# Kernel optimization log

Hardware: AMD Instinct MI355X
Metric: run time of the kernel (lower is better)

## Reference

```python
import jax, jax.numpy as jnp
import numpy as np
import math

FACTOR = 5

def setup_inputs() -> dict:
    key = jax.random.key(0)
    k1, k2, k3, k4 = jax.random.split(key, 4)
    B, L, H, D = 2, 4096, 8, 64
    sample_k = min(FACTOR * int(np.ceil(np.log(L))), L)  # 45
    return {
        "queries": jax.random.normal(k1, (B, L, H, D), dtype=jnp.float32),
        "keys": jax.random.normal(k2, (B, L, H, D), dtype=jnp.float32),
        "values": jax.random.normal(k3, (B, L, H, D), dtype=jnp.float32),
        "attn_mask": jnp.zeros((1,), dtype=bool),  # unused (mask_flag=False)
        "index_sample": jax.random.randint(k4, (L, sample_k), 0, L, dtype=jnp.int64),
    }

def reference(queries, keys, values, attn_mask, index_sample):
    B, L_Q, H, D = queries.shape
    L_K = keys.shape[1]
    # [B,L,H,D] -> [B,H,L,D]
    q = jnp.transpose(queries, (0, 2, 1, 3))
    k = jnp.transpose(keys, (0, 2, 1, 3))
    v = jnp.transpose(values, (0, 2, 1, 3))

    n_top = min(FACTOR * int(np.ceil(np.log(L_Q))), L_Q)  # u

    # --- _prob_QK ---
    # K_sample[b,h,l,s,e] = k[b,h,index_sample[l,s],e]
    K_sample = k[:, :, index_sample, :]                      # [B,H,L_Q,S,E]
    Q_K_sample = jnp.einsum('bhle,bhlse->bhls', q, K_sample)  # [B,H,L_Q,S]
    # sparsity measure: max - mean(over full L_K as in torch code)
    M = Q_K_sample.max(axis=-1) - Q_K_sample.sum(axis=-1) / L_K  # [B,H,L_Q]
    M_top = jax.lax.top_k(M, n_top)[1]                        # [B,H,u] indices

    Q_reduce = jnp.take_along_axis(q, M_top[..., None], axis=2)  # [B,H,u,E]
    scores_top = jnp.einsum('bhue,bhke->bhuk', Q_reduce, k)      # [B,H,u,L_K]

    scale = 1.0 / math.sqrt(D)
    attn = jax.nn.softmax(scale * scores_top, axis=-1)           # [B,H,u,L_K]
    context_in_q = jnp.einsum('bhuk,bhkd->bhud', attn, v)        # [B,H,u,D]

    # scatter selected contexts into zero-initialized tensor
    b_idx = jnp.arange(B)[:, None, None]
    h_idx = jnp.arange(H)[None, :, None]
    context = jnp.zeros((B, H, L_Q, D), dtype=queries.dtype)
    context = context.at[b_idx, h_idx, M_top].set(context_in_q)

    return jnp.transpose(context, (0, 2, 1, 3))  # [B,L_Q,H,D]
```

## Files before the change

kernel.cpp:

```cpp
#include <hip/hip_runtime.h>
#include <math.h>

#define B_ 2
#define L_ 4096
#define H_ 8
#define D_ 64
#define S_ 45
#define NTOP_ 45
#define SCALE 0.125f
#define TKEYS 64
#define NSPLIT 64

__global__ __launch_bounds__(256) void compute_M_kernel(
    const float* __restrict__ q, const float* __restrict__ k,
    const int* __restrict__ samp, float* __restrict__ M) {
    __shared__ int sIdx[4 * 48];
    int tid = threadIdx.x;
    int g   = blockIdx.x;
    int xcd = g & 7;
    int s0  = g >> 3;
    int b   = xcd >> 2;
    int chunk = (xcd & 3) + 4 * s0;
    int l0  = chunk * 4;

    if (tid < 4 * S_) {
        int qq = tid / S_, ss = tid - qq * S_;
        sIdx[qq * 48 + ss] = samp[(long)(l0 + qq) * S_ + ss];
    }
    if (tid < 12) sIdx[(tid / 3) * 48 + S_ + (tid % 3)] = 0;
    __syncthreads();

    int lane = tid & 63, w = tid >> 6;
    int l = l0 + w;
    int h = lane >> 3, part = lane & 7;

    const float4* qrow = (const float4*)(q + ((long)(b * L_ + l)) * (H_ * D_));
    float4 qa = qrow[2 * lane], qb = qrow[2 * lane + 1];

    const float4* kb4 = (const float4*)(k + (long)b * L_ * (H_ * D_));
    const int* myIdx = sIdx + w * 48;

    const float4* r0 = kb4 + (long)myIdx[0] * (H_ * D_ / 4);
    float4 ka0 = r0[2 * lane], kb0 = r0[2 * lane + 1];
    const float4* r1 = kb4 + (long)myIdx[1] * (H_ * D_ / 4);
    float4 ka1 = r1[2 * lane], kb1 = r1[2 * lane + 1];

    float vmax = -INFINITY, vsum = 0.f;
    #pragma unroll 3
    for (int s = 0; s < S_; ++s) {
        int nidx = myIdx[s + 2];
        const float4* nr = kb4 + (long)nidx * (H_ * D_ / 4);
        float4 na = nr[2 * lane], nb = nr[2 * lane + 1];

        float p = qa.x * ka0.x + qa.y * ka0.y + qa.z * ka0.z + qa.w * ka0.w
                + qb.x * kb0.x + qb.y * kb0.y + qb.z * kb0.z + qb.w * kb0.w;
        p += __shfl_xor(p, 1, 64);
        p += __shfl_xor(p, 2, 64);
        p += __shfl_xor(p, 4, 64);
        vmax = fmaxf(vmax, p);
        vsum += p;

        ka0 = ka1; kb0 = kb1;
        ka1 = na;  kb1 = nb;
    }
    if (part == 0)
        M[((long)(b * H_ + h)) * L_ + l] = vmax - vsum * (1.0f / (float)L_);
}

__global__ __launch_bounds__(256) void topk_kernel(
    const float* __restrict__ M, int* __restrict__ topIdx) {
    __shared__ unsigned int hist[256];
    __shared__ unsigned int suf[257];
    __shared__ unsigned int wsum[4];
    __shared__ int sBin, sRemain, sCnt, sTieCnt;
    __shared__ int tie[64];

    int bh = blockIdx.x, tid = threadIdx.x;
    int lane = tid & 63, wave = tid >> 6;
    const float* row = M + (long)bh * L_;

    unsigned int key[16];
    #pragma unroll
    for (int j = 0; j < 16; ++j) {
        unsigned int bts = __float_as_uint(row[tid + 256 * j]);
        key[j] = bts ^ ((unsigned int)((int)bts >> 31) | 0x80000000u);
    }

    unsigned int prefix = 0, pmask = 0;
    int remain = NTOP_;
    #pragma unroll 1
    for (int pass = 3; pass >= 0; --pass) {
        int shift = pass * 8;
        hist[tid] = 0;
        __syncthreads();
        #pragma unroll
        for (int j = 0; j < 16; ++j) {
            if ((key[j] & pmask) == prefix)
                atomicAdd(&hist[(key[j] >> shift) & 255u], 1u);
        }
        __syncthreads();
        unsigned int s = hist[tid];
        #pragma unroll
        for (int off = 1; off < 64; off <<= 1) {
            unsigned int o = __shfl_down(s, off, 64);
            if (lane + off < 64) s += o;
        }
        if (lane == 0) wsum[wave] = s;
        __syncthreads();
        unsigned int add = 0;
        for (int w = wave + 1; w < 4; ++w) add += wsum[w];
        s += add;
        suf[tid] = s;
        if (tid == 0) suf[256] = 0;
        __syncthreads();
        if (suf[tid] >= (unsigned int)remain && suf[tid + 1] < (unsigned int)remain) {
            sBin = tid;
            sRemain = remain - (int)suf[tid + 1];
        }
        __syncthreads();
        prefix |= ((unsigned int)sBin) << shift;
        pmask  |= 0xFFu << shift;
        remain  = sRemain;
        __syncthreads();
    }

    if (tid == 0) { sCnt = 0; sTieCnt = 0; }
    __syncthreads();
    int* outRow = topIdx + bh * NTOP_;
    #pragma unroll
    for (int j = 0; j < 16; ++j) {
        int idx = tid + 256 * j;
        if (key[j] > prefix) {
            int pos = atomicAdd(&sCnt, 1);
            outRow[pos] = idx;
        } else if (key[j] == prefix) {
            int tp = atomicAdd(&sTieCnt, 1);
            if (tp < 64) tie[tp] = idx;
        }
    }
    __syncthreads();
    if (tid == 0) {
        int base = sCnt;
        int tc = sTieCnt < 64 ? sTieCnt : 64;
        for (int t = 0; t < remain; ++t) {
            int mi = 0x7fffffff, mj = 0;
            for (int j2 = 0; j2 < tc; ++j2)
                if (tie[j2] < mi) { mi = tie[j2]; mj = j2; }
            outRow[base + t] = mi;
            tie[mj] = 0x7fffffff;
        }
    }
}

#define STRIDE 68
__global__ __launch_bounds__(256, 2) void attn_strip_kernel(
    const float* __restrict__ q, const float* __restrict__ k,
    const float* __restrict__ v, const int* __restrict__ topIdx,
    float* __restrict__ pOut, float* __restrict__ plPart, int nsplit) {
    __shared__ float sQ[48 * STRIDE];
    __shared__ float sK[TKEYS * STRIDE];
    __shared__ float sV[TKEYS * STRIDE];
    __shared__ float sP[48 * STRIDE];

    int g = blockIdx.x;
    int xcd = g & 7;
    int s0 = g >> 3;
    int grp = s0 / nsplit;
    int bh = xcd + 8 * grp;
    int split = s0 - grp * nsplit;
    int b = bh >> 3, h = bh & 7;
    int tid = threadIdx.x;
    int key0 = split * TKEYS;

    #pragma unroll
    for (int j = 0; j < 3; ++j) {
        int i = tid + 256 * j;
        int u = i >> 4, d4 = i & 15;
        float4 val = make_float4(0.f, 0.f, 0.f, 0.f);
        if (u < NTOP_) {
            int lq = topIdx[bh * NTOP_ + u];
            val = *(const float4*)(q + (((long)(b * L_ + lq)) * H_ + h) * D_ + 4 * d4);
        }
        *(float4*)(sQ + u * STRIDE + 4 * d4) = val;
    }
    #pragma unroll
    for (int j = 0; j < 4; ++j) {
        int i = tid + 256 * j;
        int r = i >> 4, d4 = i & 15;
        long off = (((long)(b * L_ + key0 + r)) * H_ + h) * D_ + 4 * d4;
        *(float4*)(sK + r * STRIDE + 4 * d4) = *(const float4*)(k + off);
        *(float4*)(sV + r * STRIDE + 4 * d4) = *(const float4*)(v + off);
    }
    __syncthreads();

    int tx = tid & 15, ty = tid >> 4;
    float acc[3][4];
    #pragma unroll
    for (int i = 0; i < 3; ++i)
        #pragma unroll
        for (int j = 0; j < 4; ++j) acc[i][j] = 0.f;

    #pragma unroll 4
    for (int d4 = 0; d4 < 16; ++d4) {
        float4 qv[3];
        #pragma unroll
        for (int i = 0; i < 3; ++i)
            qv[i] = *(const float4*)(sQ + (3 * ty + i) * STRIDE + 4 * d4);
        #pragma unroll
        for (int j = 0; j < 4; ++j) {
            float4 kv = *(const float4*)(sK + (tx + 16 * j) * STRIDE + 4 * d4);
            #pragma unroll
            for (int i = 0; i < 3; ++i)
                acc[i][j] += qv[i].x * kv.x + qv[i].y * kv.y + qv[i].z * kv.z + qv[i].w * kv.w;
        }
    }
    #pragma unroll
    for (int i = 0; i < 3; ++i) {
        #pragma unroll
        for (int j = 0; j < 4; ++j)
            sP[(3 * ty + i) * STRIDE + tx + 16 * j] = __expf(acc[i][j] * SCALE);
    }
    __syncthreads();

    int dx = tid & 15, uy = tid >> 4;
    float o[3][4];
    float ls[3];
    #pragma unroll
    for (int i = 0; i < 3; ++i) {
        ls[i] = 0.f;
        #pragma unroll
        for (int c = 0; c < 4; ++c) o[i][c] = 0.f;
    }
    #pragma unroll 4
    for (int k4 = 0; k4 < 16; ++k4) {
        float pa[3][4];
        #pragma unroll
        for (int i = 0; i < 3; ++i)
            *(float4*)pa[i] = *(const float4*)(sP + (3 * uy + i) * STRIDE + 4 * k4);
        #pragma unroll
        for (int c = 0; c < 4; ++c) {
            float4 vr = *(const float4*)(sV + (4 * k4 + c) * STRIDE + 4 * dx);
            #pragma unroll
            for (int i = 0; i < 3; ++i) {
                o[i][0] += pa[i][c] * vr.x;
                o[i][1] += pa[i][c] * vr.y;
                o[i][2] += pa[i][c] * vr.z;
                o[i][3] += pa[i][c] * vr.w;
                ls[i]   += pa[i][c];
            }
        }
    }
    #pragma unroll
    for (int i = 0; i < 3; ++i) {
        int u = 3 * uy + i;
        if (u < NTOP_) {
            long base = ((long)(split * 16 + bh) * NTOP_ + u) * D_;
            *(float4*)(pOut + base + 4 * dx) = make_float4(o[i][0], o[i][1], o[i][2], o[i][3]);
            if (dx == 0) plPart[(long)(split * 16 + bh) * NTOP_ + u] = ls[i];
        }
    }
}

__global__ __launch_bounds__(256) void reduce_norm_kernel(
    const int* __restrict__ topIdx, const float* __restrict__ pOut,
    const float* __restrict__ plPart, float* __restrict__ out, int nsplit) {
    __shared__ float part[4][64];
    __shared__ float lpart[4];
    int u = blockIdx.x, bh = blockIdx.y;
    int b = bh >> 3, h = bh & 7;
    int tid = threadIdx.x;
    int d = tid & 63, sg = tid >> 6;
    float acc = 0.f, lsum = 0.f;
    for (int s = sg; s < nsplit; s += 4) {
        acc  += pOut[((long)(s * 16 + bh) * NTOP_ + u) * D_ + d];
        lsum += plPart[(long)(s * 16 + bh) * NTOP_ + u];
    }
    part[sg][d] = acc;
    if (d == 0) lpart[sg] = lsum;
    __syncthreads();
    if (sg == 0) {
        float a = part[0][d] + part[1][d] + part[2][d] + part[3][d];
        float lt = lpart[0] + lpart[1] + lpart[2] + lpart[3];
        int lq = topIdx[bh * NTOP_ + u];
        out[(((long)(b * L_ + lq)) * H_ + h) * D_ + d] = a / lt;
    }
}

extern "C" void kernel_launch(void* const* d_in, const int* in_sizes, int n_in,
                              void* d_out, int out_size, void* d_ws, size_t ws_size,
                              hipStream_t stream) {
    const float* q = (const float*)d_in[0];
    const float* k = (const float*)d_in[1];
    const float* v = (const float*)d_in[2];
    const int* samp = (const int*)d_in[4];
    float* out = (float*)d_out;

    char* ws = (char*)d_ws;
    const size_t mBytes   = (size_t)B_ * H_ * L_ * sizeof(float);
    const size_t topBytes = (size_t)B_ * H_ * NTOP_ * sizeof(int);
    const size_t plBytes  = (size_t)NSPLIT * 16 * NTOP_ * sizeof(float);
    float* M      = (float*)ws;
    int*   topIdx = (int*)(ws + mBytes);
    float* plPart = (float*)(ws + mBytes + topBytes);
    float* pOut   = (float*)(ws + mBytes + topBytes + plBytes);

    int nsplit = NSPLIT;
    while (nsplit > 1) {
        size_t need = mBytes + topBytes + plBytes +
                      (size_t)nsplit * 16 * NTOP_ * D_ * sizeof(float);
        if (need <= ws_size) break;
        nsplit >>= 1;
    }

    hipMemsetAsync(d_out, 0, (size_t)out_size * sizeof(float), stream);

    compute_M_kernel<<<2048, 256, 0, stream>>>(q, k, samp, M);

    topk_kernel<<<B_ * H_, 256, 0, stream>>>(M, topIdx);

    attn_strip_kernel<<<nsplit * B_ * H_, 256, 0, stream>>>(
        q, k, v, topIdx, pOut, plPart, nsplit);

    dim3 gn(NTOP_, B_ * H_);
    reduce_norm_kernel<<<gn, 256, 0, stream>>>(topIdx, pOut, plPart, out, nsplit);
}
```

Baseline: 184.8 us.

## Split compute_M work across head-pairs so each wave handles two queries

Restructures the sampled QK sparsity kernel so each block covers 8 queries for one pair of heads (128 floats) rather than 4 queries across all heads. Each half-wave loads a single float4 per sampled key row instead of two and reduces over 16 lanes, and the grid doubles to 4096 blocks. The intent is more parallelism and a smaller per-thread register and load footprint, with the XCD mapping keyed to head-pair. In exchange the sample index table is loaded twice as often and each block reads narrower 512-byte segments of every key row.

```diff
diff --git a/kernel.cpp b/kernel.cpp
--- a/kernel.cpp
+++ b/kernel.cpp
@@ -14,57 +14,57 @@
 __global__ __launch_bounds__(256) void compute_M_kernel(
     const float* __restrict__ q, const float* __restrict__ k,
     const int* __restrict__ samp, float* __restrict__ M) {
-    __shared__ int sIdx[4 * 48];
+    __shared__ int sIdx[8 * 48];
     int tid = threadIdx.x;
     int g   = blockIdx.x;
     int xcd = g & 7;
-    int s0  = g >> 3;
+    int blk = g >> 3;
     int b   = xcd >> 2;
-    int chunk = (xcd & 3) + 4 * s0;
-    int l0  = chunk * 4;
-
-    if (tid < 4 * S_) {
-        int qq = tid / S_, ss = tid - qq * S_;
+    int hp  = xcd & 3;
+    int l0  = blk * 8;
+
+    for (int i = tid; i < 8 * S_; i += 256) {
+        int qq = i / S_, ss = i - qq * S_;
         sIdx[qq * 48 + ss] = samp[(long)(l0 + qq) * S_ + ss];
     }
-    if (tid < 12) sIdx[(tid / 3) * 48 + S_ + (tid % 3)] = 0;
+    if (tid < 24) sIdx[(tid / 3) * 48 + S_ + (tid % 3)] = 0;
     __syncthreads();
 
     int lane = tid & 63, w = tid >> 6;
-    int l = l0 + w;
-    int h = lane >> 3, part = lane & 7;
-
-    const float4* qrow = (const float4*)(q + ((long)(b * L_ + l)) * (H_ * D_));
-    float4 qa = qrow[2 * lane], qb = qrow[2 * lane + 1];
-
-    const float4* kb4 = (const float4*)(k + (long)b * L_ * (H_ * D_));
-    const int* myIdx = sIdx + w * 48;
-
-    const float4* r0 = kb4 + (long)myIdx[0] * (H_ * D_ / 4);
-    float4 ka0 = r0[2 * lane], kb0 = r0[2 * lane + 1];
-    const float4* r1 = kb4 + (long)myIdx[1] * (H_ * D_ / 4);
-    float4 ka1 = r1[2 * lane], kb1 = r1[2 * lane + 1];
+    int qh  = lane >> 5;
+    int i32 = lane & 31;
+    int qi  = w * 2 + qh;
+    int l   = l0 + qi;
+    int hl  = i32 >> 4;
+    int part = i32 & 15;
+
+    const float* qbase = q + ((long)(b * L_ + l)) * (H_ * D_) + hp * 128;
+    float4 qf = *(const float4*)(qbase + i32 * 4);
+
+    const float* kbase = k + (long)b * L_ * (H_ * D_) + hp * 128;
+    const int* myIdx = sIdx + qi * 48;
+
+    float4 k0 = *(const float4*)(kbase + (long)myIdx[0] * (H_ * D_) + i32 * 4);
+    float4 k1 = *(const float4*)(kbase + (long)myIdx[1] * (H_ * D_) + i32 * 4);
 
     float vmax = -INFINITY, vsum = 0.f;
-    #pragma unroll 3
+    #pragma unroll 5
     for (int s = 0; s < S_; ++s) {
         int nidx = myIdx[s + 2];
-        const float4* nr = kb4 + (long)nidx * (H_ * D_ / 4);
-        float4 na = nr[2 * lane], nb = nr[2 * lane + 1];
-
-        float p = qa.x * ka0.x + qa.y * ka0.y + qa.z * ka0.z + qa.w * ka0.w
-                + qb.x * kb0.x + qb.y * kb0.y + qb.z * kb0.z + qb.w * kb0.w;
+        float4 kn = *(const float4*)(kbase + (long)nidx * (H_ * D_) + i32 * 4);
+
+        float p = qf.x * k0.x + qf.y * k0.y + qf.z * k0.z + qf.w * k0.w;
         p += __shfl_xor(p, 1, 64);
         p += __shfl_xor(p, 2, 64);
         p += __shfl_xor(p, 4, 64);
+        p += __shfl_xor(p, 8, 64);
         vmax = fmaxf(vmax, p);
         vsum += p;
 
-        ka0 = ka1; kb0 = kb1;
-        ka1 = na;  kb1 = nb;
+        k0 = k1; k1 = kn;
     }
     if (part == 0)
-        M[((long)(b * H_ + h)) * L_ + l] = vmax - vsum * (1.0f / (float)L_);
+        M[((long)(b * H_ + hp * 2 + hl)) * L_ + l] = vmax - vsum * (1.0f / (float)L_);
 }
 
 __global__ __launch_bounds__(256) void topk_kernel(
@@ -314,7 +314,7 @@
 
     hipMemsetAsync(d_out, 0, (size_t)out_size * sizeof(float), stream);
 
-    compute_M_kernel<<<2048, 256, 0, stream>>>(q, k, samp, M);
+    compute_M_kernel<<<4096, 256, 0, stream>>>(q, k, samp, M);
 
     topk_kernel<<<B_ * H_, 256, 0, stream>>>(M, topIdx);
 
```

Result: faster. 166.3 us (-10.0%).
